# Optimization experiments

Measured on AMD Instinct MI355X. Metric: run time of the kernel, lower is better.

## Reference

```python
import jax, jax.numpy as jnp
import numpy as np

HIDDEN = 2048
HEADS = 16
HEAD_DIM = HIDDEN // HEADS  # 128
NUM_LATENTS = 16
LN_EPS = 1e-5


def setup_inputs() -> dict:
    key = jax.random.key(0)
    ks = jax.random.split(key, 16)
    B, S, D = 8, 4096, HIDDEN
    glorot = lambda k, fi, fo: jax.random.uniform(k, (fi, fo), jnp.float32,
                                                  -np.sqrt(6.0 / (fi + fo)), np.sqrt(6.0 / (fi + fo)))
    return {
        "hidden_states": jax.random.normal(ks[0], (B, S, D), jnp.float32),
        "ln_g": jnp.ones((D,), jnp.float32),
        "ln_b": jnp.zeros((D,), jnp.float32),
        "latents": 0.02 * jax.random.normal(ks[1], (NUM_LATENTS, D), jnp.float32),
        # weights stored as [in, out] (transpose of torch Linear.weight)
        "w_lq": glorot(ks[2], D, D), "b_lq": jnp.zeros((D,), jnp.float32),
        "w_k": glorot(ks[3], D, D), "b_k": jnp.zeros((D,), jnp.float32),
        "w_v": glorot(ks[4], D, D), "b_v": jnp.zeros((D,), jnp.float32),
        "w_lv": glorot(ks[5], D, D), "b_lv": jnp.zeros((D,), jnp.float32),
        "w_out": glorot(ks[6], D, D), "b_out": jnp.zeros((D,), jnp.float32),
    }


def reference(hidden_states, ln_g, ln_b, latents, w_lq, b_lq, w_k, b_k,
              w_v, b_v, w_lv, b_lv, w_out, b_out):
    x = hidden_states
    B, S, D = x.shape
    H, hd, L = HEADS, HEAD_DIM, latents.shape[0]
    # pre-LayerNorm
    mu = jnp.mean(x, axis=-1, keepdims=True)
    var = jnp.var(x, axis=-1, keepdims=True)
    h = (x - mu) / jnp.sqrt(var + LN_EPS) * ln_g + ln_b
    # projections
    k = (h @ w_k + b_k).reshape(B, S, H, hd)          # keys   [B,S,H,hd]
    v = (h @ w_v + b_v).reshape(B, S, H, hd)          # values [B,S,H,hd]
    q = (latents @ w_lq + b_lq).reshape(L, H, hd)     # latent queries [L,H,hd]
    # latent cross-attention: scores [B,H,L,S]
    scores = jnp.einsum("lhd,bshd->bhls", q, k) / np.sqrt(hd).astype(x.dtype)
    probs = jax.nn.softmax(scores, axis=-1)           # dropout is identity at eval
    ctx = jnp.einsum("bhls,bshd->blhd", probs, v).reshape(B, L, D)
    lv = ctx @ w_lv + b_lv                            # [B,L,D]
    pooled = jnp.mean(lv, axis=1, keepdims=True)      # [B,1,D]
    out = pooled @ w_out + b_out                      # [B,1,D]
    return x + jnp.broadcast_to(out, (B, S, D))       # residual add
```

## Files before the change

kernel.cpp:

```cpp
#include <hip/hip_runtime.h>
#include <hip/hip_bf16.h>

#define BB 8
#define SS 4096
#define DD 2048
#define HH 16
#define HDIM 128
#define LL 16
#define JJ 256
#define ROWS (BB*SS)
#define LN_EPS 1e-5f

typedef __attribute__((ext_vector_type(8))) short short8;
typedef __attribute__((ext_vector_type(4))) float f32x4;

typedef __attribute__((address_space(1))) const unsigned int gu32;
typedef __attribute__((address_space(3))) unsigned int lu32;
__device__ __forceinline__ void async16(const void* g, void* l) {
  __builtin_amdgcn_global_load_lds((gu32*)g, (lu32*)l, 16, 0, 0);
}

__device__ __forceinline__ unsigned short f2bf(float f) {
  unsigned int u = __builtin_bit_cast(unsigned int, f);
  u += 0x7fffu + ((u >> 16) & 1u);
  return (unsigned short)(u >> 16);
}
__device__ __forceinline__ float bf2f(unsigned short u) {
  unsigned int v = ((unsigned int)u) << 16;
  return __builtin_bit_cast(float, v);
}

__global__ __launch_bounds__(256) void k_q_part(const float* latents, const float* w_lq, float* qpart) {
  int c  = blockIdx.x * 256 + threadIdx.x;
  int e0 = blockIdx.y * 64;
  float acc[16];
#pragma unroll
  for (int l = 0; l < 16; ++l) acc[l] = 0.f;
  for (int e = e0; e < e0 + 64; ++e) {
    float w = w_lq[(size_t)e * 2048 + c];
#pragma unroll
    for (int l = 0; l < 16; ++l) acc[l] += latents[l * 2048 + e] * w;
  }
#pragma unroll
  for (int l = 0; l < 16; ++l) qpart[((size_t)blockIdx.y * 16 + l) * 2048 + c] = acc[l];
}

__global__ __launch_bounds__(256) void k_reduce(const float* part, const float* bias, float* out, int R) {
  int c = blockIdx.x * 256 + threadIdx.x;
  int r = blockIdx.y;
  float s = bias[c];
  for (int p = 0; p < 32; ++p) s += part[((size_t)p * R + r) * 2048 + c];
  out[r * 2048 + c] = s;
}

__global__ __launch_bounds__(256) void k_lnT(const float* x, const float* ln_g, const float* ln_b,
                                             short* h) {
  int row = blockIdx.x;
  int t = threadIdx.x;
  const float4* xr = (const float4*)(x + (size_t)row * 2048);
  float4 v0 = xr[t * 2];
  float4 v1 = xr[t * 2 + 1];
  float s  = v0.x + v0.y + v0.z + v0.w + v1.x + v1.y + v1.z + v1.w;
  float s2 = v0.x*v0.x + v0.y*v0.y + v0.z*v0.z + v0.w*v0.w
           + v1.x*v1.x + v1.y*v1.y + v1.z*v1.z + v1.w*v1.w;
#pragma unroll
  for (int o = 32; o; o >>= 1) { s += __shfl_down(s, o); s2 += __shfl_down(s2, o); }
  __shared__ float red[8];
  int wid = t >> 6;
  if ((t & 63) == 0) { red[wid] = s; red[4 + wid] = s2; }
  __syncthreads();
  float ts  = red[0] + red[1] + red[2] + red[3];
  float ts2 = red[4] + red[5] + red[6] + red[7];
  float mu   = ts * (1.0f / 2048.0f);
  float var  = ts2 * (1.0f / 2048.0f) - mu * mu;
  float rstd = rsqrtf(var + LN_EPS);
  const float4* gp = (const float4*)ln_g;
  const float4* bp = (const float4*)ln_b;
  float4 g0 = gp[t * 2], g1 = gp[t * 2 + 1];
  float4 b0 = bp[t * 2], b1 = bp[t * 2 + 1];
  short8 o;
  o[0] = (short)f2bf((v0.x - mu) * rstd * g0.x + b0.x);
  o[1] = (short)f2bf((v0.y - mu) * rstd * g0.y + b0.y);
  o[2] = (short)f2bf((v0.z - mu) * rstd * g0.z + b0.z);
  o[3] = (short)f2bf((v0.w - mu) * rstd * g0.w + b0.w);
  o[4] = (short)f2bf((v1.x - mu) * rstd * g1.x + b1.x);
  o[5] = (short)f2bf((v1.y - mu) * rstd * g1.y + b1.y);
  o[6] = (short)f2bf((v1.z - mu) * rstd * g1.z + b1.z);
  o[7] = (short)f2bf((v1.w - mu) * rstd * g1.w + b1.w);
  ((short8*)(h + (size_t)row * 2048))[t] = o;
}

__global__ __launch_bounds__(256) void k_wq(const float* w_k, const float* q, short* wq_t) {
  int e = blockIdx.x;
  __shared__ float wrow[2048];
  for (int i = threadIdx.x; i < 512; i += 256)
    ((float4*)wrow)[i] = ((const float4*)(w_k + (size_t)e * 2048))[i];
  __syncthreads();
  int j = threadIdx.x;
  int h = j >> 4, l = j & 15;
  const float* qrow = q + l * 2048 + h * 128;
  const float* wr = wrow + h * 128;
  float acc = 0.f;
#pragma unroll 8
  for (int d = 0; d < 128; ++d) acc += wr[d] * qrow[d];
  wq_t[(size_t)j * 2048 + e] = (short)f2bf(acc * 0.08838834764831845f);
}

__global__ __launch_bounds__(256, 3) void k_scores(const short* h, const short* wq_t,
                                                   short* scores, float* part_ms) {
  int s0 = blockIdx.x * 64;
  int jbase = blockIdx.y * 128;
  int b  = blockIdx.z;
  __shared__ short lds[2 * 12288];
  int t = threadIdx.x, lane = t & 63, w = t >> 6;
  f32x4 zero = {0.f, 0.f, 0.f, 0.f};
  f32x4 acc[2][4];
#pragma unroll
  for (int m = 0; m < 2; ++m)
#pragma unroll
    for (int n = 0; n < 4; ++n) acc[m][n] = zero;

  int rsel = t >> 3;
  int kcs  = (t & 7) ^ ((t >> 3) & 7);
  const short* hbase  = h + ((size_t)(b * 4096 + s0)) * 2048;
  const short* wqbase = wq_t + (size_t)jbase * 2048;
  int koff0 = (((lane >> 4)) ^ (lane & 7)) * 8;
  int koff1 = ((4 + (lane >> 4)) ^ (lane & 7)) * 8;

#define STAGE_SC(K0, BUF) { \
    short* lA_ = lds + (BUF) * 12288; \
    short* lB_ = lA_ + 8192; \
    _Pragma("unroll") \
    for (int i_ = 0; i_ < 4; ++i_) \
      async16(wqbase + (size_t)(i_ * 32 + rsel) * 2048 + (K0) + kcs * 8, lA_ + (i_ * 256 + t) * 8); \
    _Pragma("unroll") \
    for (int i_ = 0; i_ < 2; ++i_) \
      async16(hbase + (size_t)(i_ * 32 + rsel) * 2048 + (K0) + kcs * 8, lB_ + (i_ * 256 + t) * 8); \
  }

  int cur = 0;
  STAGE_SC(0, 0);
  for (int it = 0; it < 32; ++it) {
    if (it < 31) {
      STAGE_SC((it + 1) * 64, cur ^ 1);
      asm volatile("s_waitcnt vmcnt(6)" ::: "memory");
    } else {
      asm volatile("s_waitcnt vmcnt(0)" ::: "memory");
    }
    __builtin_amdgcn_s_barrier();
    __builtin_amdgcn_sched_barrier(0);
    const short* lA = lds + cur * 12288;
    const short* lB = lA + 8192;
#pragma unroll
    for (int kk = 0; kk < 2; ++kk) {
      int ko = kk ? koff1 : koff0;
      short8 afr[2];
#pragma unroll
      for (int m = 0; m < 2; ++m)
        afr[m] = *(const short8*)(lA + (w * 32 + m * 16 + (lane & 15)) * 64 + ko);
#pragma unroll
      for (int n = 0; n < 4; ++n) {
        short8 bfr = *(const short8*)(lB + (n * 16 + (lane & 15)) * 64 + ko);
#pragma unroll
        for (int m = 0; m < 2; ++m)
          acc[m][n] = __builtin_amdgcn_mfma_f32_16x16x32_bf16(afr[m], bfr, acc[m][n], 0, 0, 0);
      }
    }
    __builtin_amdgcn_s_barrier();
    cur ^= 1;
  }
#undef STAGE_SC

  int hi = lane >> 4, cc = lane & 15;
#pragma unroll
  for (int m = 0; m < 2; ++m) {
#pragma unroll
    for (int i = 0; i < 4; ++i) {
      int j = jbase + w * 32 + m * 16 + hi * 4 + i;
      float v[4];
#pragma unroll
      for (int n = 0; n < 4; ++n) {
        unsigned short u = f2bf(acc[m][n][i]);
        scores[((size_t)(b * 256 + j)) * 4096 + s0 + n * 16 + cc] = (short)u;
        v[n] = bf2f(u);
      }
      float mx = fmaxf(fmaxf(v[0], v[1]), fmaxf(v[2], v[3]));
#pragma unroll
      for (int o = 1; o < 16; o <<= 1) mx = fmaxf(mx, __shfl_xor(mx, o));
      float sm = __expf(v[0] - mx) + __expf(v[1] - mx) + __expf(v[2] - mx) + __expf(v[3] - mx);
#pragma unroll
      for (int o = 1; o < 16; o <<= 1) sm += __shfl_xor(sm, o);
      if (cc == 0)
        ((float2*)part_ms)[((size_t)(b * 256 + j)) * 64 + blockIdx.x] = make_float2(mx, sm);
    }
  }
}

__global__ __launch_bounds__(256) void k_pt(const short* scores, const float* part_ms,
                                            const short* h, float* Tpart) {
  int sp = blockIdx.x;
  int b  = blockIdx.y;
  int eh = blockIdx.z;
  int t  = threadIdx.x;
  __shared__ short sc[256 * 128];
  __shared__ float lp[16 * 128];
  __shared__ float lms[512];
  {
    const float2* p = ((const float2*)part_ms) + (size_t)(b * 256 + t) * 64;
    float M = -1e30f;
#pragma unroll 8
    for (int i = 0; i < 64; ++i) M = fmaxf(M, p[i].x);
    float S = 0.f;
#pragma unroll 8
    for (int i = 0; i < 64; ++i) S += p[i].y * __expf(p[i].x - M);
    lms[t * 2] = M; lms[t * 2 + 1] = 1.0f / (16.0f * S);
  }
#pragma unroll
  for (int rr = 0; rr < 2; ++rr) {
    int j = rr * 128 + (t >> 1);
    const short8* src = (const short8*)(scores + ((size_t)(b * 256 + j)) * 4096 + sp * 128 + (t & 1) * 64);
    short8* dst = (short8*)(sc + j * 128 + (t & 1) * 64);
#pragma unroll
    for (int i = 0; i < 8; ++i) dst[i] = src[i];
  }
  __syncthreads();
  {
    int s = t & 127, hg = (t >> 7) * 8;
    for (int hh = hg; hh < hg + 8; ++hh) {
      float accp = 0.f;
#pragma unroll
      for (int l = 0; l < 16; ++l) {
        int r = hh * 16 + l;
        accp += __expf(bf2f((unsigned short)sc[r * 128 + s]) - lms[r * 2]) * lms[r * 2 + 1];
      }
      lp[hh * 128 + s] = accp;
    }
  }
  __syncthreads();
  f32x4 a[16];
#pragma unroll
  for (int hh = 0; hh < 16; ++hh) a[hh] = (f32x4){0.f, 0.f, 0.f, 0.f};
  int e0 = eh * 1024 + t * 4;
  const short* hb = h + ((size_t)(b * 4096 + sp * 128)) * 2048 + e0;
  for (int si = 0; si < 128; ++si) {
    short4 hv4 = *(const short4*)(hb + (size_t)si * 2048);
    float hv[4];
    hv[0] = bf2f((unsigned short)hv4.x); hv[1] = bf2f((unsigned short)hv4.y);
    hv[2] = bf2f((unsigned short)hv4.z); hv[3] = bf2f((unsigned short)hv4.w);
#pragma unroll
    for (int hh = 0; hh < 16; ++hh) {
      float p = lp[hh * 128 + si];
#pragma unroll
      for (int c = 0; c < 4; ++c) a[hh][c] += p * hv[c];
    }
  }
#pragma unroll
  for (int hh = 0; hh < 16; ++hh)
    *(f32x4*)(Tpart + ((size_t)(sp * 128 + b * 16 + hh)) * 2048 + e0) = a[hh];
}

__global__ __launch_bounds__(256) void k_cbar_part(const float* Tpart, const float* w_v, float* part) {
  int t  = threadIdx.x;
  int c  = blockIdx.x * 256 + t;
  int e0 = blockIdx.y * 64;
  __shared__ float tb[2][8][64];
  {
    int idx = t * 4;
    int hl = idx >> 9, b = (idx >> 6) & 7, ee = idx & 63;
    int hg = blockIdx.x * 2 + hl;
    f32x4 s = {0.f, 0.f, 0.f, 0.f};
    for (int sp = 0; sp < 32; ++sp) {
      f32x4 v = *(const f32x4*)(Tpart + ((size_t)(sp * 128 + b * 16 + hg)) * 2048 + e0 + ee);
      s += v;
    }
    *(f32x4*)&tb[hl][b][ee] = s;
  }
  __syncthreads();
  int h1 = t >> 7;
  float acc[8];
#pragma unroll
  for (int b = 0; b < 8; ++b) acc[b] = 0.f;
  for (int e = 0; e < 64; ++e) {
    float wv = w_v[(size_t)(e0 + e) * 2048 + c];
#pragma unroll
    for (int b = 0; b < 8; ++b) acc[b] += tb[h1][b][e] * wv;
  }
#pragma unroll
  for (int b = 0; b < 8; ++b) part[((size_t)blockIdx.y * 8 + b) * 2048 + c] = acc[b];
}

__global__ __launch_bounds__(256) void k_vecmat_part(const float* partin, const float* bias,
                                                     const float* W, float* partout) {
  int t  = threadIdx.x;
  int c  = blockIdx.x * 256 + t;
  int e0 = blockIdx.y * 64;
  __shared__ float vin[8][64];
  {
#pragma unroll
    for (int k = 0; k < 2; ++k) {
      int idx = t * 2 + k;
      int b = idx >> 6, ee = idx & 63;
      float s = bias[e0 + ee];
      for (int p = 0; p < 32; ++p) s += partin[((size_t)p * 8 + b) * 2048 + e0 + ee];
      vin[b][ee] = s;
    }
  }
  __syncthreads();
  float acc[8];
#pragma unroll
  for (int b = 0; b < 8; ++b) acc[b] = 0.f;
  for (int e = 0; e < 64; ++e) {
    float wv = W[(size_t)(e0 + e) * 2048 + c];
#pragma unroll
    for (int b = 0; b < 8; ++b) acc[b] += vin[b][e] * wv;
  }
#pragma unroll
  for (int b = 0; b < 8; ++b) partout[((size_t)blockIdx.y * 8 + b) * 2048 + c] = acc[b];
}

__global__ __launch_bounds__(256) void k_resid(const float* x, const float* outv, float* out) {
  size_t i4 = (size_t)blockIdx.x * 256 + threadIdx.x;
  size_t total4 = (size_t)ROWS * 512;
  size_t stride = (size_t)gridDim.x * 256;
  for (; i4 < total4; i4 += stride) {
    int b  = (int)(i4 >> 21);
    int c4 = (int)(i4 & 511);
    float4 xv = ((const float4*)x)[i4];
    float4 ov = ((const float4*)outv)[b * 512 + c4];
    float4 o;
    o.x = xv.x + ov.x; o.y = xv.y + ov.y;
    o.z = xv.z + ov.z; o.w = xv.w + ov.w;
    ((float4*)out)[i4] = o;
  }
}

extern "C" void kernel_launch(void* const* d_in, const int* in_sizes, int n_in,
                              void* d_out, int out_size, void* d_ws, size_t ws_size,
                              hipStream_t stream) {
  const float* x       = (const float*)d_in[0];
  const float* ln_g    = (const float*)d_in[1];
  const float* ln_b    = (const float*)d_in[2];
  const float* latents = (const float*)d_in[3];
  const float* w_lq    = (const float*)d_in[4];
  const float* b_lq    = (const float*)d_in[5];
  const float* w_k     = (const float*)d_in[6];
  const float* w_v     = (const float*)d_in[8];
  const float* b_v     = (const float*)d_in[9];
  const float* w_lv    = (const float*)d_in[10];
  const float* b_lv    = (const float*)d_in[11];
  const float* w_out   = (const float*)d_in[12];
  const float* b_out   = (const float*)d_in[13];

  char* base = (char*)d_out;
  short* scores  = (short*)(base);
  short* h       = (short*)(base + 16777216);
  float* Tpart   = (float*)(base + 150994944);
  float* part_ms = (float*)(base + 184549376);
  float* q       = (float*)(base + 185597952);
  short* wq_t    = (short*)(base + 185729024);
  float* qpart   = (float*)(base + 186777600);
  float* part    = (float*)(base + 190971904);
  float* part2   = (float*)(base + 193069056);
  float* outv    = (float*)d_ws;
  float* out     = (float*)d_out;

  k_q_part     <<<dim3(8, 32), 256, 0, stream>>>(latents, w_lq, qpart);
  k_reduce     <<<dim3(8, 16), 256, 0, stream>>>(qpart, b_lq, q, 16);
  k_lnT        <<<32768, 256, 0, stream>>>(x, ln_g, ln_b, h);
  k_wq         <<<2048, 256, 0, stream>>>(w_k, q, wq_t);
  k_scores     <<<dim3(64, 2, 8), 256, 0, stream>>>(h, wq_t, scores, part_ms);
  k_pt         <<<dim3(32, 8, 2), 256, 0, stream>>>(scores, part_ms, h, Tpart);
  k_cbar_part  <<<dim3(8, 32), 256, 0, stream>>>(Tpart, w_v, part);
  k_vecmat_part<<<dim3(8, 32), 256, 0, stream>>>(part, b_v, w_lv, part2);
  k_vecmat_part<<<dim3(8, 32), 256, 0, stream>>>(part2, b_lv, w_out, part);
  k_reduce     <<<dim3(8, 8), 256, 0, stream>>>(part, b_out, outv, 8);
  k_resid      <<<2048, 256, 0, stream>>>(x, outv, out);
}
```

Baseline: 431.4 us.

## Retile k_pt to 64-row sequence chunks with full-width 8-element columns per thread

The probability-weighted h reduction kernel now processes 64 sequence positions per block over the full 2048-wide feature dimension, instead of 128 positions over half of it. Each thread loads 8 bf16 values per row and reads its probabilities with vectorized LDS loads from a transposed, padded lp layout. Scores are no longer loaded once per feature half, and the grid stays at 512 blocks. In exchange the Tpart partial buffer doubles, so the downstream reduction sums 64 partials instead of 32, scratch offsets move, and each thread holds 128 accumulators, which raises register pressure.

```diff
diff --git a/kernel.cpp b/kernel.cpp
--- a/kernel.cpp
+++ b/kernel.cpp
@@ -200,10 +200,9 @@
                                             const short* h, float* Tpart) {
   int sp = blockIdx.x;
   int b  = blockIdx.y;
-  int eh = blockIdx.z;
   int t  = threadIdx.x;
-  __shared__ short sc[256 * 128];
-  __shared__ float lp[16 * 128];
+  __shared__ short sc[256 * 64];
+  __shared__ __align__(16) float lp[64 * 20];
   __shared__ float lms[512];
   {
     const float2* p = ((const float2*)part_ms) + (size_t)(b * 256 + t) * 64;
@@ -215,48 +214,62 @@
     for (int i = 0; i < 64; ++i) S += p[i].y * __expf(p[i].x - M);
     lms[t * 2] = M; lms[t * 2 + 1] = 1.0f / (16.0f * S);
   }
-#pragma unroll
-  for (int rr = 0; rr < 2; ++rr) {
-    int j = rr * 128 + (t >> 1);
-    const short8* src = (const short8*)(scores + ((size_t)(b * 256 + j)) * 4096 + sp * 128 + (t & 1) * 64);
-    short8* dst = (short8*)(sc + j * 128 + (t & 1) * 64);
+  {
+    const short8* src = (const short8*)(scores + ((size_t)(b * 256 + t)) * 4096 + sp * 64);
+    short8* dst = (short8*)(sc + t * 64);
 #pragma unroll
     for (int i = 0; i < 8; ++i) dst[i] = src[i];
   }
   __syncthreads();
   {
-    int s = t & 127, hg = (t >> 7) * 8;
-    for (int hh = hg; hh < hg + 8; ++hh) {
+    int s = t & 63, hg = (t >> 6) * 4;
+    for (int hh = hg; hh < hg + 4; ++hh) {
       float accp = 0.f;
 #pragma unroll
       for (int l = 0; l < 16; ++l) {
         int r = hh * 16 + l;
-        accp += __expf(bf2f((unsigned short)sc[r * 128 + s]) - lms[r * 2]) * lms[r * 2 + 1];
+        accp += __expf(bf2f((unsigned short)sc[r * 64 + s]) - lms[r * 2]) * lms[r * 2 + 1];
       }
-      lp[hh * 128 + s] = accp;
-    }
-  }
-  __syncthreads();
-  f32x4 a[16];
-#pragma unroll
-  for (int hh = 0; hh < 16; ++hh) a[hh] = (f32x4){0.f, 0.f, 0.f, 0.f};
-  int e0 = eh * 1024 + t * 4;
-  const short* hb = h + ((size_t)(b * 4096 + sp * 128)) * 2048 + e0;
-  for (int si = 0; si < 128; ++si) {
-    short4 hv4 = *(const short4*)(hb + (size_t)si * 2048);
-    float hv[4];
-    hv[0] = bf2f((unsigned short)hv4.x); hv[1] = bf2f((unsigned short)hv4.y);
-    hv[2] = bf2f((unsigned short)hv4.z); hv[3] = bf2f((unsigned short)hv4.w);
-#pragma unroll
-    for (int hh = 0; hh < 16; ++hh) {
-      float p = lp[hh * 128 + si];
-#pragma unroll
-      for (int c = 0; c < 4; ++c) a[hh][c] += p * hv[c];
-    }
-  }
-#pragma unroll
-  for (int hh = 0; hh < 16; ++hh)
-    *(f32x4*)(Tpart + ((size_t)(sp * 128 + b * 16 + hh)) * 2048 + e0) = a[hh];
+      lp[s * 20 + hh] = accp;
+    }
+  }
+  __syncthreads();
+  f32x4 a[16][2];
+#pragma unroll
+  for (int hh = 0; hh < 16; ++hh) { a[hh][0] = (f32x4){0,0,0,0}; a[hh][1] = (f32x4){0,0,0,0}; }
+  int e0 = t * 8;
+  const short* hb = h + ((size_t)(b * 4096 + sp * 64)) * 2048 + e0;
+  for (int si = 0; si < 64; ++si) {
+    short8 hv8 = *(const short8*)(hb + (size_t)si * 2048);
+    float hv[8];
+#pragma unroll
+    for (int c = 0; c < 8; ++c) hv[c] = bf2f((unsigned short)hv8[c]);
+    f32x4 p0 = *(const f32x4*)(lp + si * 20);
+    f32x4 p1 = *(const f32x4*)(lp + si * 20 + 4);
+    f32x4 p2 = *(const f32x4*)(lp + si * 20 + 8);
+    f32x4 p3 = *(const f32x4*)(lp + si * 20 + 12);
+#pragma unroll
+    for (int q4 = 0; q4 < 4; ++q4) {
+      float pv = q4 == 0 ? p0[0] : q4 == 1 ? p0[1] : q4 == 2 ? p0[2] : p0[3];
+    }
+#pragma unroll
+    for (int k4 = 0; k4 < 4; ++k4) {
+      float pa = p0[k4], pb = p1[k4], pc = p2[k4], pd = p3[k4];
+#pragma unroll
+      for (int c = 0; c < 4; ++c) {
+        a[k4][0][c]      += pa * hv[c];  a[k4][1][c]      += pa * hv[4 + c];
+        a[4 + k4][0][c]  += pb * hv[c];  a[4 + k4][1][c]  += pb * hv[4 + c];
+        a[8 + k4][0][c]  += pc * hv[c];  a[8 + k4][1][c]  += pc * hv[4 + c];
+        a[12 + k4][0][c] += pd * hv[c];  a[12 + k4][1][c] += pd * hv[4 + c];
+      }
+    }
+  }
+#pragma unroll
+  for (int hh = 0; hh < 16; ++hh) {
+    float* dst = Tpart + ((size_t)(sp * 128 + b * 16 + hh)) * 2048 + e0;
+    *(f32x4*)dst = a[hh][0];
+    *(f32x4*)(dst + 4) = a[hh][1];
+  }
 }
 
 __global__ __launch_bounds__(256) void k_cbar_part(const float* Tpart, const float* w_v, float* part) {
@@ -269,7 +282,7 @@
     int hl = idx >> 9, b = (idx >> 6) & 7, ee = idx & 63;
     int hg = blockIdx.x * 2 + hl;
     f32x4 s = {0.f, 0.f, 0.f, 0.f};
-    for (int sp = 0; sp < 32; ++sp) {
+    for (int sp = 0; sp < 64; ++sp) {
       f32x4 v = *(const f32x4*)(Tpart + ((size_t)(sp * 128 + b * 16 + hg)) * 2048 + e0 + ee);
       s += v;
     }
@@ -355,12 +368,12 @@
   short* scores  = (short*)(base);
   short* h       = (short*)(base + 16777216);
   float* Tpart   = (float*)(base + 150994944);
-  float* part_ms = (float*)(base + 184549376);
-  float* q       = (float*)(base + 185597952);
-  short* wq_t    = (short*)(base + 185729024);
-  float* qpart   = (float*)(base + 186777600);
-  float* part    = (float*)(base + 190971904);
-  float* part2   = (float*)(base + 193069056);
+  float* part_ms = (float*)(base + 218103808);
+  float* q       = (float*)(base + 219152384);
+  short* wq_t    = (short*)(base + 219283456);
+  float* qpart   = (float*)(base + 220332032);
+  float* part    = (float*)(base + 224526336);
+  float* part2   = (float*)(base + 226623488);
   float* outv    = (float*)d_ws;
   float* out     = (float*)d_out;
 
@@ -369,7 +382,7 @@
   k_lnT        <<<32768, 256, 0, stream>>>(x, ln_g, ln_b, h);
   k_wq         <<<2048, 256, 0, stream>>>(w_k, q, wq_t);
   k_scores     <<<dim3(64, 2, 8), 256, 0, stream>>>(h, wq_t, scores, part_ms);
-  k_pt         <<<dim3(32, 8, 2), 256, 0, stream>>>(scores, part_ms, h, Tpart);
+  k_pt         <<<dim3(64, 8), 256, 0, stream>>>(scores, part_ms, h, Tpart);
   k_cbar_part  <<<dim3(8, 32), 256, 0, stream>>>(Tpart, w_v, part);
   k_vecmat_part<<<dim3(8, 32), 256, 0, stream>>>(part, b_v, w_lv, part2);
   k_vecmat_part<<<dim3(8, 32), 256, 0, stream>>>(part2, b_lv, w_out, part);
```

Measured after the change: 438.8 us. Within noise of the previous version (+1.7%).
